# Kernel optimization log

Hardware: AMD Instinct MI355X
Metric: run time of the kernel (lower is better)

## Reference

```python
import jax, jax.numpy as jnp
import numpy as np

N = 50000
E = 800000
F_IN = 128
HID = 128
NCLS = 40


def setup_inputs() -> dict:
    key = jax.random.key(0)
    ks = jax.random.split(key, 12)
    def glorot(k, fan_in, fan_out):
        s = jnp.sqrt(6.0 / (fan_in + fan_out))
        return jax.random.uniform(k, (fan_in, fan_out), jnp.float32, -s, s)
    x = jax.random.normal(ks[0], (N, F_IN), jnp.float32)
    edge_index = jax.random.randint(ks[1], (2, E), 0, N, jnp.int64)
    W1 = glorot(ks[2], F_IN, HID); b1 = jnp.zeros((HID,), jnp.float32)
    W2 = glorot(ks[3], HID, HID);  b2 = jnp.zeros((HID,), jnp.float32)
    W3 = glorot(ks[4], HID, HID);  b3 = jnp.zeros((HID,), jnp.float32)
    Wc = glorot(ks[5], HID, NCLS)
    bc = jnp.zeros((NCLS,), jnp.float32)
    return {"x": x, "edge_index": edge_index, "W1": W1, "b1": b1,
            "W2": W2, "b2": b2, "W3": W3, "b3": b3, "Wc": Wc, "bc": bc}


def _gcn_conv(h, src, dst, norm, W, b):
    # GCNConv: linear transform, then normalized scatter-add aggregation
    h = h @ W                              # [N, out]
    msg = h[src] * norm[:, None]           # [E+N, out] gathered + scaled
    out = jax.ops.segment_sum(msg, dst, num_segments=N)
    return out + b


def reference(x, edge_index, W1, b1, W2, b2, W3, b3, Wc, bc):
    # add self-loops (PyG GCNConv default) and compute symmetric norm once
    loop = jnp.arange(N, dtype=edge_index.dtype)
    src = jnp.concatenate([edge_index[0], loop])
    dst = jnp.concatenate([edge_index[1], loop])
    deg = jax.ops.segment_sum(jnp.ones_like(dst, dtype=x.dtype), dst, num_segments=N)
    dinv = jax.lax.rsqrt(deg)              # deg >= 1 due to self-loops
    norm = dinv[src] * dinv[dst]           # [E+N]

    h = jax.nn.relu(_gcn_conv(x, src, dst, norm, W1, b1))
    h = jax.nn.relu(_gcn_conv(h, src, dst, norm, W2, b2))
    h = jax.nn.relu(_gcn_conv(h, src, dst, norm, W3, b3))
    out = h @ Wc + bc
    return (out, h)
```

## Files before the change

### kernel.cpp

```cpp
#include <hip/hip_runtime.h>
#include <hip/hip_fp16.h>


#define FEAT 128

typedef _Float16 half_t;
typedef _Float16 f16x8 __attribute__((ext_vector_type(8)));
typedef float f32x16 __attribute__((ext_vector_type(16)));


__global__ __launch_bounds__(256) void k_prep(const float* __restrict__ W1,
                                              const float* __restrict__ W2,
                                              const float* __restrict__ W3,
                                              half_t* __restrict__ Wt1,
                                              half_t* __restrict__ Wt2,
                                              half_t* __restrict__ Wt3,
                                              int* __restrict__ deg, int N) {
  int idx = blockIdx.x * 256 + threadIdx.x;
  if (idx < N) deg[idx] = 0;
  if (idx < 3 * 16384) {
    int which = idx >> 14;
    int i = idx & 16383;
    int k = i >> 7, n = i & 127;
    const float* W = (which == 0) ? W1 : (which == 1) ? W2 : W3;
    half_t* Wt = (which == 0) ? Wt1 : (which == 1) ? Wt2 : Wt3;
    Wt[n * 128 + k] = (half_t)W[i];
  }
}


__global__ __launch_bounds__(256) void k_count_rank(const int* __restrict__ dst,
                                                    int* __restrict__ deg,
                                                    int* __restrict__ rank, int E) {
  int e = blockIdx.x * 256 + threadIdx.x;
  if (e < E) rank[e] = atomicAdd(&deg[dst[e]], 1);
}

__global__ __launch_bounds__(256) void k_scanA(const int* __restrict__ deg,
                                               int* __restrict__ partial, int N) {
  __shared__ int s[256];
  int t = threadIdx.x;
  int i = blockIdx.x * 256 + t;
  s[t] = (i < N) ? deg[i] : 0;
  __syncthreads();
  for (int off = 128; off > 0; off >>= 1) {
    if (t < off) s[t] += s[t + off];
    __syncthreads();
  }
  if (t == 0) partial[blockIdx.x] = s[0];
}

__global__ __launch_bounds__(256) void k_scanB(int* __restrict__ partial, int nblk,
                                               int* __restrict__ offsets, int N) {
  __shared__ int s[256];
  int t = threadIdx.x;
  int v = (t < nblk) ? partial[t] : 0;
  s[t] = v;
  __syncthreads();
  for (int off = 1; off < 256; off <<= 1) {
    int x = (t >= off) ? s[t - off] : 0;
    __syncthreads();
    s[t] += x;
    __syncthreads();
  }
  if (t < nblk) partial[t] = s[t] - v;
  if (t == 0) offsets[N] = s[255];
}

__global__ __launch_bounds__(256) void k_scanC(const int* __restrict__ deg,
                                               const int* __restrict__ partial,
                                               int* __restrict__ offsets,
                                               float* __restrict__ dinv, int N) {
  __shared__ int s[256];
  int t = threadIdx.x;
  int i = blockIdx.x * 256 + t;
  int v = (i < N) ? deg[i] : 0;
  s[t] = v;
  __syncthreads();
  for (int off = 1; off < 256; off <<= 1) {
    int x = (t >= off) ? s[t - off] : 0;
    __syncthreads();
    s[t] += x;
    __syncthreads();
  }
  if (i < N) {
    offsets[i] = partial[blockIdx.x] + s[t] - v;
    dinv[i] = rsqrtf((float)(v + 1));
  }
}

__global__ __launch_bounds__(256) void k_place(const int* __restrict__ src,
                                               const int* __restrict__ dst,
                                               const int* __restrict__ offsets,
                                               const int* __restrict__ rank,
                                               unsigned short* __restrict__ col,
                                               int E) {
  int e = blockIdx.x * 256 + threadIdx.x;
  if (e < E) col[offsets[dst[e]] + rank[e]] = (unsigned short)src[e];
}

template <int SRC_FP32>
__global__ __launch_bounds__(256) void k_gemm_mfma(const void* __restrict__ Asrc,
                                                   const half_t* __restrict__ Wt,
                                                   const float* __restrict__ dinv,
                                                   half_t* __restrict__ T,
                                                   int nrows) {
  __shared__ char lds[65536];
  char* sA = lds;
  char* sW = lds + 32768;
  int t = threadIdx.x;
  int rowBase = blockIdx.x * 128;
  int rowsHere = min(128, nrows - rowBase);

  #pragma unroll
  for (int i = 0; i < 8; ++i) {
    int lin = t + i * 256;
    int r = lin >> 4, c = lin & 15;
    *(float4*)(sW + r * 256 + ((c * 16) ^ ((r & 15) << 4))) =
        *(const float4*)((const char*)Wt + r * 256 + c * 16);
  }
  if (SRC_FP32) {
    const float* Af = (const float*)Asrc;
    #pragma unroll
    for (int i = 0; i < 8; ++i) {
      int lin = t + i * 256;
      int r = lin >> 4, c = lin & 15;
      f16x8 h = {};
      if (r < rowsHere) {
        const float4* p = (const float4*)(Af + (size_t)(rowBase + r) * FEAT + c * 8);
        float4 v0 = p[0], v1 = p[1];
        h[0] = (half_t)v0.x; h[1] = (half_t)v0.y; h[2] = (half_t)v0.z; h[3] = (half_t)v0.w;
        h[4] = (half_t)v1.x; h[5] = (half_t)v1.y; h[6] = (half_t)v1.z; h[7] = (half_t)v1.w;
      }
      *(f16x8*)(sA + r * 256 + ((c * 16) ^ ((r & 15) << 4))) = h;
    }
  } else {
    const char* Ah = (const char*)Asrc;
    #pragma unroll
    for (int i = 0; i < 8; ++i) {
      int lin = t + i * 256;
      int r = lin >> 4, c = lin & 15;
      float4 v = {};
      if (r < rowsHere) v = *(const float4*)(Ah + (size_t)(rowBase + r) * 256 + c * 16);
      *(float4*)(sA + r * 256 + ((c * 16) ^ ((r & 15) << 4))) = v;
    }
  }
  __syncthreads();

  int wv = t >> 6;
  int l = t & 63;
  int l31 = l & 31;
  int lhi = l >> 5;
  int sw = (l31 & 15) << 4;

  f32x16 acc[4] = {};

  #pragma unroll
  for (int step = 0; step < 8; ++step) {
    int ko = (step * 32 + lhi * 16) ^ sw;
    f16x8 a  = *(const f16x8*)(sA + (wv * 32 + l31) * 256 + ko);
    f16x8 b0 = *(const f16x8*)(sW + (l31) * 256 + ko);
    f16x8 b1 = *(const f16x8*)(sW + (32 + l31) * 256 + ko);
    f16x8 b2 = *(const f16x8*)(sW + (64 + l31) * 256 + ko);
    f16x8 b3 = *(const f16x8*)(sW + (96 + l31) * 256 + ko);
    acc[0] = __builtin_amdgcn_mfma_f32_32x32x16_f16(a, b0, acc[0], 0, 0, 0);
    acc[1] = __builtin_amdgcn_mfma_f32_32x32x16_f16(a, b1, acc[1], 0, 0, 0);
    acc[2] = __builtin_amdgcn_mfma_f32_32x32x16_f16(a, b2, acc[2], 0, 0, 0);
    acc[3] = __builtin_amdgcn_mfma_f32_32x32x16_f16(a, b3, acc[3], 0, 0, 0);
  }

  #pragma unroll
  for (int j = 0; j < 16; ++j) {
    int rloc = wv * 32 + (j & 3) + 8 * (j >> 2) + 4 * lhi;
    if (rloc < rowsHere) {
      int grow = rowBase + rloc;
      float d = dinv[grow];
      #pragma unroll
      for (int n = 0; n < 4; ++n) {
        T[(size_t)grow * FEAT + n * 32 + l31] = (half_t)(acc[n][j] * d);
      }
    }
  }
}

template <int OUTF>
__global__ __launch_bounds__(256) void k_aggregate(const uint2* __restrict__ T4,
                                                   const int* __restrict__ offsets,
                                                   const unsigned short* __restrict__ col,
                                                   const float* __restrict__ dinv,
                                                   const float* __restrict__ bias,
                                                   float4* __restrict__ outF,
                                                   uint2* __restrict__ outH,
                                                   int N) {
  int wave = threadIdx.x >> 6;
  int half = (threadIdx.x >> 5) & 1;
  int q = threadIdx.x & 31;
  int node = (blockIdx.x * 4 + wave) * 2 + half;
  if (node >= N) return;
  int e0 = offsets[node], e1 = offsets[node + 1];

  uint2 sv = T4[(size_t)node * 32 + q];
  __half2 h0 = *(__half2*)&sv.x, h1 = *(__half2*)&sv.y;
  float ax = __half2float(h0.x), ay = __half2float(h0.y);
  float az = __half2float(h1.x), aw = __half2float(h1.y);

  int e = e0;
  for (; e + 8 <= e1; e += 8) {
    int s0 = col[e + 0], s1 = col[e + 1], s2 = col[e + 2], s3 = col[e + 3];
    int s4 = col[e + 4], s5 = col[e + 5], s6 = col[e + 6], s7 = col[e + 7];
    uint2 v0 = T4[(size_t)s0 * 32 + q];
    uint2 v1 = T4[(size_t)s1 * 32 + q];
    uint2 v2 = T4[(size_t)s2 * 32 + q];
    uint2 v3 = T4[(size_t)s3 * 32 + q];
    uint2 v4 = T4[(size_t)s4 * 32 + q];
    uint2 v5 = T4[(size_t)s5 * 32 + q];
    uint2 v6 = T4[(size_t)s6 * 32 + q];
    uint2 v7 = T4[(size_t)s7 * 32 + q];
    #pragma unroll
    for (int u = 0; u < 8; ++u) {
      uint2 v = (u == 0) ? v0 : (u == 1) ? v1 : (u == 2) ? v2 : (u == 3) ? v3
              : (u == 4) ? v4 : (u == 5) ? v5 : (u == 6) ? v6 : v7;
      __half2 p0 = *(__half2*)&v.x, p1 = *(__half2*)&v.y;
      ax += __half2float(p0.x); ay += __half2float(p0.y);
      az += __half2float(p1.x); aw += __half2float(p1.y);
    }
  }
  for (; e < e1; ++e) {
    uint2 v = T4[(size_t)col[e] * 32 + q];
    __half2 p0 = *(__half2*)&v.x, p1 = *(__half2*)&v.y;
    ax += __half2float(p0.x); ay += __half2float(p0.y);
    az += __half2float(p1.x); aw += __half2float(p1.y);
  }

  float di = dinv[node];
  float4 b = ((const float4*)bias)[q];
  float ox = fmaxf(di * ax + b.x, 0.f);
  float oy = fmaxf(di * ay + b.y, 0.f);
  float oz = fmaxf(di * az + b.z, 0.f);
  float ow = fmaxf(di * aw + b.w, 0.f);
  if (OUTF) {
    outF[(size_t)node * 32 + q] = make_float4(ox, oy, oz, ow);
  } else {
    uint2 o;
    __half2 t0 = __floats2half2_rn(ox, oy), t1 = __floats2half2_rn(oz, ow);
    o.x = *(unsigned*)&t0; o.y = *(unsigned*)&t1;
    outH[(size_t)node * 32 + q] = o;
  }
}

__global__ __launch_bounds__(256) void k_classifier(const float* __restrict__ h,
                                                    const float* __restrict__ Wc,
                                                    const float* __restrict__ bc,
                                                    float* __restrict__ out, int N) {
  __shared__ float sh[64 * 132];
  __shared__ float sWt[40 * 130];
  int t = threadIdx.x;
  int nodeBase = blockIdx.x * 64;
  int nodesHere = min(64, N - nodeBase);

  for (int i = t; i < FEAT * 40; i += 256) {
    int k = i / 40, c = i - k * 40;
    sWt[c * 130 + k] = Wc[i];
  }
  {
    const float4* H4 = (const float4*)(h + (size_t)nodeBase * FEAT);
    #pragma unroll
    for (int i = 0; i < 8; ++i) {
      int lin = t + i * 256;
      int r = lin >> 5, kc = lin & 31;
      float4 v = make_float4(0.f, 0.f, 0.f, 0.f);
      if (r < nodesHere) v = H4[lin];
      *(float4*)&sh[r * 132 + kc * 4] = v;
    }
  }
  __syncthreads();

  int n0 = (t >> 3) * 2;
  int cg = (t & 7) * 5;
  float acc0[5], acc1[5];
  #pragma unroll
  for (int j = 0; j < 5; ++j) { acc0[j] = bc[cg + j]; acc1[j] = acc0[j]; }

  #pragma unroll 4
  for (int k4 = 0; k4 < 32; ++k4) {
    float4 h0 = *(const float4*)&sh[n0 * 132 + k4 * 4];
    float4 h1 = *(const float4*)&sh[(n0 + 1) * 132 + k4 * 4];
    #pragma unroll
    for (int j = 0; j < 5; ++j) {
      float4 w = *(const float4*)&sWt[(cg + j) * 130 + k4 * 4];
      acc0[j] += h0.x * w.x + h0.y * w.y + h0.z * w.z + h0.w * w.w;
      acc1[j] += h1.x * w.x + h1.y * w.y + h1.z * w.z + h1.w * w.w;
    }
  }

  if (n0 < nodesHere) {
    float* o = out + (size_t)(nodeBase + n0) * 40 + cg;
    #pragma unroll
    for (int j = 0; j < 5; ++j) o[j] = acc0[j];
  }
  if (n0 + 1 < nodesHere) {
    float* o = out + (size_t)(nodeBase + n0 + 1) * 40 + cg;
    #pragma unroll
    for (int j = 0; j < 5; ++j) o[j] = acc1[j];
  }
}


extern "C" void kernel_launch(void* const* d_in, const int* in_sizes, int n_in,
                              void* d_out, int out_size, void* d_ws, size_t ws_size,
                              hipStream_t stream) {
  const float* x    = (const float*)d_in[0];
  const int*   edge = (const int*)d_in[1];
  const float* W1   = (const float*)d_in[2];
  const float* b1   = (const float*)d_in[3];
  const float* W2   = (const float*)d_in[4];
  const float* b2   = (const float*)d_in[5];
  const float* W3   = (const float*)d_in[6];
  const float* b3   = (const float*)d_in[7];
  const float* Wc   = (const float*)d_in[8];
  const float* bc   = (const float*)d_in[9];

  int N = in_sizes[0] / FEAT;
  int E = in_sizes[1] / 2;

  float* out  = (float*)d_out;
  float* hOut = out + (size_t)N * 40;

  size_t o = 0;
  char* wsb = (char*)d_ws;
  auto take = [&](size_t bytes) -> void* {
    void* p = wsb + o;
    o += (bytes + 255) & ~(size_t)255;
    return p;
  };
  float*          dinv    = (float*)take((size_t)N * 4);
  int*            deg     = (int*)take((size_t)N * 4);
  int*            rank    = (int*)take((size_t)E * 4);
  int*            partial = (int*)take(256 * 4);
  int*            offsets = (int*)take(((size_t)N + 8) * 4);
  unsigned short* col     = (unsigned short*)take((size_t)E * 2);
  half_t*         T2h     = (half_t*)take((size_t)N * FEAT * 2);
  half_t*         Bh      = (half_t*)take((size_t)N * FEAT * 2);
  half_t*         Wt1     = (half_t*)take(16384 * 2);
  half_t*         Wt2     = (half_t*)take(16384 * 2);
  half_t*         Wt3     = (half_t*)take(16384 * 2);

  const int* e_src = edge;
  const int* e_dst = edge + E;

  int nblk = (N + 255) / 256;
  int eblk = (E + 255) / 256;

  k_prep<<<nblk, 256, 0, stream>>>(W1, W2, W3, Wt1, Wt2, Wt3, deg, N);
  k_count_rank<<<eblk, 256, 0, stream>>>(e_dst, deg, rank, E);
  k_scanA<<<nblk, 256, 0, stream>>>(deg, partial, N);
  k_scanB<<<1, 256, 0, stream>>>(partial, nblk, offsets, N);
  k_scanC<<<nblk, 256, 0, stream>>>(deg, partial, offsets, dinv, N);
  k_place<<<eblk, 256, 0, stream>>>(e_src, e_dst, offsets, rank, col, E);

  int gblk = (N + 127) / 128;
  int ablk = (N + 7) / 8;
  uint2* T4 = (uint2*)T2h;
  k_gemm_mfma<1><<<gblk, 256, 0, stream>>>(x, Wt1, dinv, T2h, N);
  k_aggregate<0><<<ablk, 256, 0, stream>>>(T4, offsets, col, dinv, b1, nullptr,
                                           (uint2*)Bh, N);
  k_gemm_mfma<0><<<gblk, 256, 0, stream>>>(Bh, Wt2, dinv, T2h, N);
  k_aggregate<0><<<ablk, 256, 0, stream>>>(T4, offsets, col, dinv, b2, nullptr,
                                           (uint2*)Bh, N);
  k_gemm_mfma<0><<<gblk, 256, 0, stream>>>(Bh, Wt3, dinv, T2h, N);
  k_aggregate<1><<<ablk, 256, 0, stream>>>(T4, offsets, col, dinv, b3,
                                           (float4*)hOut, nullptr, N);
  k_classifier<<<(N + 63) / 64, 256, 0, stream>>>(hOut, Wc, bc, out, N);
}
```

Before: 229.3 us.

## Slice transformed features into column blocks to shrink aggregation gather working set

The GEMM now writes its fp16 output in 8 column slices of 16 features each (32 bytes per node per slice) instead of row-major 256-byte rows. The aggregation kernel is re-gridded so each block handles one slice for 32 nodes, with 8 threads per node gathering 4 bytes each. The intent is that the gathered data per slice (about 1.6 MB) stays resident in L2 and the random neighbor gathers hit cache more often. In exchange each gather is only 32 bytes, and the col/offset reads are repeated 8 times across slices, with more blocks launched. The GEMM store also becomes a scattered 2-byte write pattern, and the code depends on the kernel's nrows matching N.

After: 253.7 us. 10.6% more time.

```diff
diff --git a/kernel.cpp b/kernel.cpp
--- a/kernel.cpp
+++ b/kernel.cpp
@@ -177,74 +177,80 @@
       float d = dinv[grow];
       #pragma unroll
       for (int n = 0; n < 4; ++n) {
-        T[(size_t)grow * FEAT + n * 32 + l31] = (half_t)(acc[n][j] * d);
+        int slice = n * 2 + (l31 >> 4);
+        T[((size_t)slice * nrows + grow) * 16 + (l31 & 15)] =
+            (half_t)(acc[n][j] * d);
       }
     }
   }
 }
 
 template <int OUTF>
-__global__ __launch_bounds__(256) void k_aggregate(const uint2* __restrict__ T4,
+__global__ __launch_bounds__(256) void k_aggregate(const unsigned* __restrict__ T32,
                                                    const int* __restrict__ offsets,
                                                    const unsigned short* __restrict__ col,
                                                    const float* __restrict__ dinv,
                                                    const float* __restrict__ bias,
-                                                   float4* __restrict__ outF,
-                                                   uint2* __restrict__ outH,
+                                                   unsigned* __restrict__ outH,
+                                                   float2* __restrict__ outF,
                                                    int N) {
-  int wave = threadIdx.x >> 6;
-  int half = (threadIdx.x >> 5) & 1;
-  int q = threadIdx.x & 31;
-  int node = (blockIdx.x * 4 + wave) * 2 + half;
+  int s = blockIdx.x & 7;
+  int grp = blockIdx.x >> 3;
+  int t = threadIdx.x;
+  int node = grp * 32 + (t >> 3);
+  int r = t & 7;
   if (node >= N) return;
+  const unsigned* Ts = T32 + (size_t)s * N * 8;
+
+  unsigned sv = Ts[(size_t)node * 8 + r];
+  __half2 p = *(__half2*)&sv;
+  float ax = __half2float(p.x), ay = __half2float(p.y);
+
   int e0 = offsets[node], e1 = offsets[node + 1];
-
-  uint2 sv = T4[(size_t)node * 32 + q];
-  __half2 h0 = *(__half2*)&sv.x, h1 = *(__half2*)&sv.y;
-  float ax = __half2float(h0.x), ay = __half2float(h0.y);
-  float az = __half2float(h1.x), aw = __half2float(h1.y);
-
   int e = e0;
   for (; e + 8 <= e1; e += 8) {
-    int s0 = col[e + 0], s1 = col[e + 1], s2 = col[e + 2], s3 = col[e + 3];
-    int s4 = col[e + 4], s5 = col[e + 5], s6 = col[e + 6], s7 = col[e + 7];
-    uint2 v0 = T4[(size_t)s0 * 32 + q];
-    uint2 v1 = T4[(size_t)s1 * 32 + q];
-    uint2 v2 = T4[(size_t)s2 * 32 + q];
-    uint2 v3 = T4[(size_t)s3 * 32 + q];
-    uint2 v4 = T4[(size_t)s4 * 32 + q];
-    uint2 v5 = T4[(size_t)s5 * 32 + q];
-    uint2 v6 = T4[(size_t)s6 * 32 + q];
-    uint2 v7 = T4[(size_t)s7 * 32 + q];
-    #pragma unroll
-    for (int u = 0; u < 8; ++u) {
-      uint2 v = (u == 0) ? v0 : (u == 1) ? v1 : (u == 2) ? v2 : (u == 3) ? v3
-              : (u == 4) ? v4 : (u == 5) ? v5 : (u == 6) ? v6 : v7;
-      __half2 p0 = *(__half2*)&v.x, p1 = *(__half2*)&v.y;
-      ax += __half2float(p0.x); ay += __half2float(p0.y);
-      az += __half2float(p1.x); aw += __half2float(p1.y);
-    }
+    int c0 = col[e + 0], c1 = col[e + 1], c2 = col[e + 2], c3 = col[e + 3];
+    int c4 = col[e + 4], c5 = col[e + 5], c6 = col[e + 6], c7 = col[e + 7];
+    unsigned v0 = Ts[(size_t)c0 * 8 + r];
+    unsigned v1 = Ts[(size_t)c1 * 8 + r];
+    unsigned v2 = Ts[(size_t)c2 * 8 + r];
+    unsigned v3 = Ts[(size_t)c3 * 8 + r];
+    unsigned v4 = Ts[(size_t)c4 * 8 + r];
+    unsigned v5 = Ts[(size_t)c5 * 8 + r];
+    unsigned v6 = Ts[(size_t)c6 * 8 + r];
+    unsigned v7 = Ts[(size_t)c7 * 8 + r];
+    __half2 q0 = *(__half2*)&v0, q1 = *(__half2*)&v1;
+    __half2 q2 = *(__half2*)&v2, q3 = *(__half2*)&v3;
+    __half2 q4 = *(__half2*)&v4, q5 = *(__half2*)&v5;
+    __half2 q6 = *(__half2*)&v6, q7 = *(__half2*)&v7;
+    float x01 = __half2float(q0.x) + __half2float(q1.x);
+    float x23 = __half2float(q2.x) + __half2float(q3.x);
+    float x45 = __half2float(q4.x) + __half2float(q5.x);
+    float x67 = __half2float(q6.x) + __half2float(q7.x);
+    float y01 = __half2float(q0.y) + __half2float(q1.y);
+    float y23 = __half2float(q2.y) + __half2float(q3.y);
+    float y45 = __half2float(q4.y) + __half2float(q5.y);
+    float y67 = __half2float(q6.y) + __half2float(q7.y);
+    ax += (x01 + x23) + (x45 + x67);
+    ay += (y01 + y23) + (y45 + y67);
   }
   for (; e < e1; ++e) {
-    uint2 v = T4[(size_t)col[e] * 32 + q];
-    __half2 p0 = *(__half2*)&v.x, p1 = *(__half2*)&v.y;
-    ax += __half2float(p0.x); ay += __half2float(p0.y);
-    az += __half2float(p1.x); aw += __half2float(p1.y);
+    unsigned v = Ts[(size_t)col[e] * 8 + r];
+    __half2 q = *(__half2*)&v;
+    ax += __half2float(q.x);
+    ay += __half2float(q.y);
   }
 
   float di = dinv[node];
-  float4 b = ((const float4*)bias)[q];
+  int w = s * 8 + r;
+  float2 b = ((const float2*)bias)[w];
   float ox = fmaxf(di * ax + b.x, 0.f);
   float oy = fmaxf(di * ay + b.y, 0.f);
-  float oz = fmaxf(di * az + b.z, 0.f);
-  float ow = fmaxf(di * aw + b.w, 0.f);
   if (OUTF) {
-    outF[(size_t)node * 32 + q] = make_float4(ox, oy, oz, ow);
+    outF[(size_t)node * 64 + w] = make_float2(ox, oy);
   } else {
-    uint2 o;
-    __half2 t0 = __floats2half2_rn(ox, oy), t1 = __floats2half2_rn(oz, ow);
-    o.x = *(unsigned*)&t0; o.y = *(unsigned*)&t1;
-    outH[(size_t)node * 32 + q] = o;
+    __half2 h = __floats2half2_rn(ox, oy);
+    outH[(size_t)node * 64 + w] = *(unsigned*)&h;
   }
 }
 
@@ -359,16 +365,16 @@
   k_place<<<eblk, 256, 0, stream>>>(e_src, e_dst, offsets, rank, col, E);
 
   int gblk = (N + 127) / 128;
-  int ablk = (N + 7) / 8;
-  uint2* T4 = (uint2*)T2h;
+  int agrp = (N + 31) / 32;
+  unsigned* T32 = (unsigned*)T2h;
   k_gemm_mfma<1><<<gblk, 256, 0, stream>>>(x, Wt1, dinv, T2h, N);
-  k_aggregate<0><<<ablk, 256, 0, stream>>>(T4, offsets, col, dinv, b1, nullptr,
-                                           (uint2*)Bh, N);
+  k_aggregate<0><<<agrp * 8, 256, 0, stream>>>(T32, offsets, col, dinv, b1,
+                                               (unsigned*)Bh, nullptr, N);
   k_gemm_mfma<0><<<gblk, 256, 0, stream>>>(Bh, Wt2, dinv, T2h, N);
-  k_aggregate<0><<<ablk, 256, 0, stream>>>(T4, offsets, col, dinv, b2, nullptr,
-                                           (uint2*)Bh, N);
+  k_aggregate<0><<<agrp * 8, 256, 0, stream>>>(T32, offsets, col, dinv, b2,
+                                               (unsigned*)Bh, nullptr, N);
   k_gemm_mfma<0><<<gblk, 256, 0, stream>>>(Bh, Wt3, dinv, T2h, N);
-  k_aggregate<1><<<ablk, 256, 0, stream>>>(T4, offsets, col, dinv, b3,
-                                           (float4*)hOut, nullptr, N);
+  k_aggregate<1><<<agrp * 8, 256, 0, stream>>>(T32, offsets, col, dinv, b3,
+                                               nullptr, (float2*)hOut, N);
   k_classifier<<<(N + 63) / 64, 256, 0, stream>>>(hOut, Wc, bc, out, N);
 }
```
